# Performance work log

Measured on AMD Instinct MI355X. Metric: run time of the kernel, lower is better.

## Reference

```python
import jax, jax.numpy as jnp
import numpy as np

EPS = 1e-5
N, CIN, C = 8192, 64, 128
K_POS, K_LARGE, K_DOWN = 16, 127, 16

def _bn(h, g, b):
    # training-mode BatchNorm1d (biased var), as in the torch forward
    return (h - h.mean(0)) / jnp.sqrt(h.var(0) + EPS) * g + b

def _knn_idx(f, k):
    # k nearest neighbors per row (self excluded), grouped per target node
    sq = jnp.sum(f * f, axis=1)
    d = sq[:, None] + sq[None, :] - 2.0 * (f @ f.T)
    d = d.at[jnp.diag_indices(f.shape[0])].set(jnp.inf)
    return jax.lax.top_k(-d, k)[1]

def _fps(pos, m):
    # farthest point sampling, deterministic start at node 0; indices are non-diff
    pos = jax.lax.stop_gradient(pos)
    n = pos.shape[0]
    def step(carry, _):
        dist, last = carry
        dist = jnp.minimum(dist, jnp.sum((pos - pos[last]) ** 2, axis=1))
        nxt = jnp.argmax(dist).astype(jnp.int32)
        return (dist, nxt), nxt
    (_, _), rest = jax.lax.scan(step, (jnp.full((n,), jnp.inf), jnp.array(0, jnp.int32)), None, length=m - 1)
    return jnp.sort(jnp.concatenate([jnp.zeros((1,), jnp.int32), rest]))

def _lin(k, i, o):
    return jax.random.normal(k, (i, o), dtype=jnp.float32) / np.float32(np.sqrt(i))

def setup_inputs():
    ks = jax.random.split(jax.random.key(0), 16)
    return dict(
        x=jax.random.normal(ks[0], (N, CIN), dtype=jnp.float32),
        pos=jax.random.uniform(ks[1], (N, 3), dtype=jnp.float32),
        edge_index=jax.random.randint(ks[2], (2, N * 16), 0, N),
        Wd=_lin(ks[3], CIN, C), bd=jnp.zeros((C,)),
        gamma_d=jnp.ones((C,)), beta_d=jnp.zeros((C,)),
        Wg1=_lin(ks[4], C, C), bg1=jnp.zeros((C,)),
        gamma_g=jnp.ones((C,)), beta_g=jnp.zeros((C,)),
        Wg2=_lin(ks[5], C, 20), bg2=jnp.zeros((20,)),
        Wlin=_lin(ks[6], C, C), Wsrc=_lin(ks[7], C, C), Wdst=_lin(ks[8], C, C),
        Wp=_lin(ks[9], 3, C), bp=jnp.zeros((C,)),
        Wa1=_lin(ks[10], C, C), ba1=jnp.zeros((C,)),
        gamma_a=jnp.ones((C,)), beta_a=jnp.zeros((C,)),
        Wa2=_lin(ks[11], C, C), ba2=jnp.zeros((C,)),
        Wu=_lin(ks[12], C, C), bu=jnp.zeros((C,)),
    )

def reference(x, pos, edge_index, Wd, bd, gamma_d, beta_d, Wg1, bg1, gamma_g, beta_g,
              Wg2, bg2, Wlin, Wsrc, Wdst, Wp, bp, Wa1, ba1, gamma_a, beta_a, Wa2, ba2, Wu, bu):
    # ---- downlayer: Linear+BN+ReLU, neighbor max-pool (w/ self loop), FPS ----
    h = jax.nn.relu(_bn(x @ Wd + bd, gamma_d, beta_d))                 # [N,C]
    pooled = jax.ops.segment_max(h[edge_index[0]], edge_index[1], num_segments=N)
    pooled = jnp.maximum(pooled, h)                                     # add self loop
    idx = _fps(pos, N // 2)
    x1, pos1 = pooled[idx], pos[idx]                                    # [M,C],[M,3]
    M = N // 2
    # ---- generate_graph: pos kNN (k=16) + feature kNN (k=127) + gumbel top-k ----
    nn_pos = _knn_idx(pos1, K_POS)                                      # [M,16]
    e_pos_src = nn_pos.reshape(-1)
    e_pos_dst = jnp.repeat(jnp.arange(M), K_POS)
    nn_feat = _knn_idx(x1, K_LARGE)                                     # [M,127]
    src_l = nn_feat.reshape(-1)
    dst_l = jnp.repeat(jnp.arange(M), K_LARGE)
    hg = jax.nn.relu(_bn(x1 @ Wg1 + bg1, gamma_g, beta_g))
    emb = hg @ Wg2 + bg2                                                # [M,20]
    k1, k2 = jax.random.split(jax.random.key(42))
    emb = emb + jax.random.uniform(k1, emb.shape) * 1e-4
    dist = jnp.linalg.norm(emb[src_l] - emb[dst_l], axis=1)
    p = jnp.exp(-(dist ** 2)).reshape(M, K_LARGE)                       # t = 1.0
    g = -jnp.log(-jnp.log(jax.random.uniform(k2, p.shape) + 1e-20) + 1e-20)
    top_i = jax.lax.top_k(jnp.log(p + 1e-20) + g, K_DOWN)[1]            # [M,16]
    flat = (top_i + jnp.arange(M)[:, None] * K_LARGE).reshape(-1)
    s = jnp.concatenate([src_l[flat], e_pos_src])                       # [E=M*32]
    d = jnp.concatenate([dst_l[flat], e_pos_dst])
    # ---- PointTransformerConv + linear_up + residual ----
    a_src, a_dst, v = x1 @ Wsrc, x1 @ Wdst, x1 @ Wlin
    delta = (pos1[d] - pos1[s]) @ Wp + bp                               # [E,C]
    alpha = a_dst[d] - a_src[s] + delta
    alpha = jax.nn.relu(_bn(alpha @ Wa1 + ba1, gamma_a, beta_a)) @ Wa2 + ba2
    amax = jax.ops.segment_max(alpha, d, num_segments=M)                # per-target softmax
    ea = jnp.exp(alpha - amax[d])
    w = ea / (jax.ops.segment_sum(ea, d, num_segments=M)[d] + 1e-16)
    out = jax.ops.segment_sum(w * (v[s] + delta), d, num_segments=M)    # [M,C]
    return out @ Wu + bu + x1
```

## Files before the change

kernel.cpp:

```cpp
#include <hip/hip_runtime.h>
#include <cstdint>
#include <cstddef>
#include <math.h>

#define NNODE 8192
#define CINP 64
#define CC 128
#define MM 4096
#define KPOS 16
#define KLARGE 127
#define KDOWN 16
#define EG (MM*KDOWN)
#define ETOT (EG*2)
#define NEDGE 131072

__host__ __device__ static inline void tf_block(uint32_t k0, uint32_t k1,
                                                uint32_t c0, uint32_t c1,
                                                uint32_t& o0, uint32_t& o1) {
  uint32_t ks2 = k0 ^ k1 ^ 0x1BD11BDAu;
  uint32_t x0 = c0 + k0, x1 = c1 + k1;
#define TFR(r) { x0 += x1; x1 = (x1 << (r)) | (x1 >> (32 - (r))); x1 ^= x0; }
  TFR(13) TFR(15) TFR(26) TFR(6)
  x0 += k1;  x1 += ks2 + 1u;
  TFR(17) TFR(29) TFR(16) TFR(24)
  x0 += ks2; x1 += k0 + 2u;
  TFR(13) TFR(15) TFR(26) TFR(6)
  x0 += k0;  x1 += k1 + 3u;
  TFR(17) TFR(29) TFR(16) TFR(24)
  x0 += k1;  x1 += ks2 + 4u;
  TFR(13) TFR(15) TFR(26) TFR(6)
  x0 += ks2; x1 += k0 + 5u;
#undef TFR
  o0 = x0; o1 = x1;
}

__global__ void k_uniform(float* __restrict__ u, int n, uint32_t ka, uint32_t kb) {
  int i = blockIdx.x * 256 + threadIdx.x;
  if (i >= n) return;
  uint32_t o0, o1;
  tf_block(ka, kb, 0u, (uint32_t)i, o0, o1);
  uint32_t bits = o0 ^ o1;
  u[i] = __uint_as_float((bits >> 9) | 0x3f800000u) - 1.0f;
}

__global__ __launch_bounds__(256) void k_gemm32(const float* __restrict__ A, const float* __restrict__ B,
                                                const float* __restrict__ bias, float* __restrict__ Cmat, int rows) {
  int id = blockIdx.x * 256 + threadIdx.x;
  int r = id >> 7, c = id & (CC - 1);
  if (r >= rows) return;
  const float* a = A + r * CC;
  float acc = 0.f;
#pragma unroll 8
  for (int k = 0; k < CC; k++) acc = __fmaf_rn(a[k], B[k * CC + c], acc);
  if (bias) acc = __fadd_rn(acc, bias[c]);
  Cmat[id] = acc;
}

template<int K>
__global__ __launch_bounds__(256) void k_gemm64(const float* __restrict__ A, const float* __restrict__ B,
                                                const float* __restrict__ bias, float* __restrict__ Cmat, int rows) {
  int id = blockIdx.x * 256 + threadIdx.x;
  int r = id >> 7, c = id & (CC - 1);
  if (r >= rows) return;
  const float* a = A + r * K;
  double acc = 0.0;
#pragma unroll 4
  for (int k = 0; k < K; k++) acc += (double)a[k] * (double)B[k * CC + c];
  float v = (float)acc;
  if (bias) v = __fadd_rn(v, bias[c]);
  Cmat[id] = v;
}

__global__ __launch_bounds__(256) void k_gemm_res(const float* __restrict__ A, const float* __restrict__ B,
                                                  const float* __restrict__ bias, const float* __restrict__ res,
                                                  float* __restrict__ Cmat, int rows) {
  int id = blockIdx.x * 256 + threadIdx.x;
  int r = id >> 7, c = id & (CC - 1);
  if (r >= rows) return;
  const float* a = A + r * CC;
  float acc = 0.f;
#pragma unroll 8
  for (int k = 0; k < CC; k++) acc = __fmaf_rn(a[k], B[k * CC + c], acc);
  acc = __fadd_rn(acc, bias[c]);
  Cmat[id] = __fadd_rn(acc, res[id]);
}

__global__ __launch_bounds__(128) void k_colsum_part(const float* __restrict__ A, int rows, int rpb,
                                                     double* __restrict__ part) {
  int c = threadIdx.x, b = blockIdx.x;
  int r0 = b * rpb, r1 = r0 + rpb; if (r1 > rows) r1 = rows;
  double s = 0.0;
  for (int r = r0; r < r1; r++) s += (double)A[(size_t)r * CC + c];
  part[(size_t)b * CC + c] = s;
}
__global__ __launch_bounds__(128) void k_colmean(const double* __restrict__ part, int np, double rows,
                                                 float* __restrict__ mean) {
  int c = threadIdx.x;
  double s = 0.0;
  for (int b = 0; b < np; b++) s += part[(size_t)b * CC + c];
  mean[c] = (float)(s / rows);
}
__global__ __launch_bounds__(128) void k_colvar_part(const float* __restrict__ A, int rows, int rpb,
                                                     const float* __restrict__ mean, double* __restrict__ part) {
  int c = threadIdx.x, b = blockIdx.x;
  int r0 = b * rpb, r1 = r0 + rpb; if (r1 > rows) r1 = rows;
  float m32 = mean[c];
  double q = 0.0;
  for (int r = r0; r < r1; r++) {
    float d = __fsub_rn(A[(size_t)r * CC + c], m32);
    q += (double)d * (double)d;
  }
  part[(size_t)b * CC + c] = q;
}
__global__ __launch_bounds__(128) void k_colvar_fin(const double* __restrict__ part, int np, double rows,
                                                    float* __restrict__ var) {
  int c = threadIdx.x;
  double s = 0.0;
  for (int b = 0; b < np; b++) s += part[(size_t)b * CC + c];
  var[c] = (float)(s / rows);
}

__global__ __launch_bounds__(128) void k_colstat64(const float* __restrict__ A, int rows, int rpb,
                                                   double* __restrict__ dsum, double* __restrict__ dsq) {
  int c = threadIdx.x;
  int r0 = blockIdx.x * rpb;
  int r1 = r0 + rpb; if (r1 > rows) r1 = rows;
  double s = 0.0, q = 0.0;
  for (int r = r0; r < r1; r++) {
    float v = A[(size_t)r * CC + c];
    s += (double)v;
    q += (double)v * (double)v;
  }
  atomicAdd(&dsum[c], s);
  atomicAdd(&dsq[c], q);
}

__global__ __launch_bounds__(128) void k_finstat(const double* __restrict__ dsum, const double* __restrict__ dsq,
                                                 double rows, float* __restrict__ mean, float* __restrict__ var) {
  int c = threadIdx.x;
  double m = dsum[c] / rows;
  mean[c] = (float)m;
  var[c] = (float)(dsq[c] / rows - m * m);
}

__global__ void k_bnrelu(const float* __restrict__ in, const float* __restrict__ mean, const float* __restrict__ var,
                         const float* __restrict__ g, const float* __restrict__ b,
                         float* __restrict__ o1, float* __restrict__ o2, int total) {
  int id = blockIdx.x * 256 + threadIdx.x;
  if (id >= total) return;
  int c = id & (CC - 1);
  float sd = __fsqrt_rn(__fadd_rn(var[c], 1e-5f));
  float vv = __fdiv_rn(__fsub_rn(in[id], mean[c]), sd);
  vv = fmaxf(__fadd_rn(__fmul_rn(vv, g[c]), b[c]), 0.0f);
  o1[id] = vv;
  if (o2) o2[id] = vv;
}

__global__ void k_pool(const float* __restrict__ h, const int* __restrict__ ei, float* __restrict__ pooled) {
  int id = blockIdx.x * 256 + threadIdx.x;
  int e = id >> 7, c = id & (CC - 1);
  int src = ei[e], dst = ei[NEDGE + e];
  atomicMax((int*)(pooled + (size_t)dst * CC + c), __float_as_int(h[(size_t)src * CC + c]));
}

#define FPS_DPP_STEP(CTRL)                                                              \
  {                                                                                     \
    uint32_t nlo = (uint32_t)__builtin_amdgcn_update_dpp(0, (int)klo, CTRL, 0xf, 0xf, true); \
    uint32_t nhi = (uint32_t)__builtin_amdgcn_update_dpp(0, (int)khi, CTRL, 0xf, 0xf, true); \
    unsigned long long nk = ((unsigned long long)nhi << 32) | nlo;                      \
    unsigned long long ck = ((unsigned long long)khi << 32) | klo;                      \
    if (nk > ck) { klo = nlo; khi = nhi; }                                              \
  }

__global__ __launch_bounds__(512) void k_fps(const float* __restrict__ pos, int* __restrict__ idx) {
  constexpr int T = 512, P = 16;
  __shared__ unsigned int keys[NNODE];
  __shared__ float ldx[NNODE], ldy[NNODE], ldz[NNODE];
  __shared__ unsigned int sel[NNODE / 32];
  __shared__ int scn[T];
  __shared__ __align__(16) unsigned long long redk[2][8];
  int t = threadIdx.x;
  for (int i = t; i < NNODE; i += T) {
    float X = pos[3 * i], Y = pos[3 * i + 1], Z = pos[3 * i + 2];
    ldx[i] = X; ldy[i] = Y; ldz[i] = Z;
    int cx = (int)(X * 64.0f); cx = cx < 0 ? 0 : (cx > 63 ? 63 : cx);
    int cy = (int)(Y * 64.0f); cy = cy < 0 ? 0 : (cy > 63 ? 63 : cy);
    int cz = (int)(Z * 64.0f); cz = cz < 0 ? 0 : (cz > 63 ? 63 : cz);
    unsigned int code = 0;
    for (int b = 0; b < 6; b++) {
      code |= (unsigned)((cx >> b) & 1) << (3 * b + 2);
      code |= (unsigned)((cy >> b) & 1) << (3 * b + 1);
      code |= (unsigned)((cz >> b) & 1) << (3 * b);
    }
    keys[i] = (code << 13) | (unsigned)i;
  }
  for (int i = t; i < NNODE / 32; i += T) sel[i] = 0u;
  __syncthreads();
  for (int k = 2; k <= NNODE; k <<= 1) {
    for (int j = k >> 1; j > 0; j >>= 1) {
      for (int i = t; i < NNODE; i += T) {
        int l = i ^ j;
        if (l > i) {
          unsigned a = keys[i], b = keys[l];
          bool up = ((i & k) == 0);
          if ((a > b) == up) { keys[i] = b; keys[l] = a; }
        }
      }
      __syncthreads();
    }
  }
  float px[P], py[P], pz[P], dist[P];
  uint32_t invo[P];
  float bnx = 1e30f, bxx = -1e30f, bny = 1e30f, bxy = -1e30f, bnz = 1e30f, bxz = -1e30f;
#pragma unroll
  for (int j = 0; j < P; j++) {
    int i = (int)(keys[t * P + j] & 8191u);
    invo[j] = (uint32_t)(8191 - i);
    px[j] = ldx[i]; py[j] = ldy[i]; pz[j] = ldz[i];
    dist[j] = __int_as_float(0x7f800000);
    bnx = fminf(bnx, px[j]); bxx = fmaxf(bxx, px[j]);
    bny = fminf(bny, py[j]); bxy = fmaxf(bxy, py[j]);
    bnz = fminf(bnz, pz[j]); bxz = fmaxf(bxz, pz[j]);
  }
  if (t == 0) sel[0] = 1u;
  float Lx = ldx[0], Ly = ldy[0], Lz = ldz[0];
  float myMax = __int_as_float(0x7f800000);
  unsigned long long myKey = 0ull;
  int w = t >> 6, lane = t & 63;
  for (int it = 0; it < MM - 1; it++) {
    float cx = fminf(fmaxf(Lx, bnx), bxx);
    float cy = fminf(fmaxf(Ly, bny), bxy);
    float cz = fminf(fmaxf(Lz, bnz), bxz);
    float ddx = Lx - cx, ddy = Ly - cy, ddz = Lz - cz;
    float lb = ddx * ddx + ddy * ddy + ddz * ddz;
    if (lb * 0.98f - 1e-6f < myMax) {
      unsigned long long bk = 0ull;
#pragma unroll
      for (int j = 0; j < P; j++) {
        float dx = __fsub_rn(px[j], Lx), dy = __fsub_rn(py[j], Ly), dz = __fsub_rn(pz[j], Lz);
        float d2 = __fadd_rn(__fadd_rn(__fmul_rn(dx, dx), __fmul_rn(dy, dy)), __fmul_rn(dz, dz));
        float nd = fminf(dist[j], d2);
        dist[j] = nd;
        unsigned long long kj = ((unsigned long long)__float_as_uint(nd) << 13) | (unsigned long long)invo[j];
        if (kj > bk) bk = kj;
      }
      myKey = bk;
      myMax = __uint_as_float((uint32_t)(bk >> 13));
    }
    uint32_t klo = (uint32_t)myKey, khi = (uint32_t)(myKey >> 32);
    FPS_DPP_STEP(0x111)
    FPS_DPP_STEP(0x112)
    FPS_DPP_STEP(0x114)
    FPS_DPP_STEP(0x118)
    FPS_DPP_STEP(0x142)
    FPS_DPP_STEP(0x143)
    uint32_t wlo = (uint32_t)__builtin_amdgcn_readlane((int)klo, 63);
    uint32_t whi = (uint32_t)__builtin_amdgcn_readlane((int)khi, 63);
    unsigned long long wk = ((unsigned long long)whi << 32) | wlo;
    int p = it & 1;
    if (lane == 0) redk[p][w] = wk;
    __syncthreads();
    const ulonglong2* rp = (const ulonglong2*)&redk[p][0];
    ulonglong2 r0 = rp[0], r1 = rp[1], r2 = rp[2], r3 = rp[3];
    unsigned long long m0 = r0.x > r0.y ? r0.x : r0.y;
    unsigned long long m1 = r1.x > r1.y ? r1.x : r1.y;
    unsigned long long m2 = r2.x > r2.y ? r2.x : r2.y;
    unsigned long long m3 = r3.x > r3.y ? r3.x : r3.y;
    unsigned long long ga = m0 > m1 ? m0 : m1;
    unsigned long long gb = m2 > m3 ? m2 : m3;
    unsigned long long g = ga > gb ? ga : gb;
    int o = 8191 - (int)(g & 8191ull);
    Lx = ldx[o]; Ly = ldy[o]; Lz = ldz[o];
    if (t == 0) atomicOr((int*)&sel[o >> 5], (int)(1u << (o & 31)));
  }
  __syncthreads();
  int cnt = 0;
#pragma unroll
  for (int j = 0; j < P; j++) {
    int i = t * P + j;
    cnt += (int)((sel[i >> 5] >> (i & 31)) & 1u);
  }
  scn[t] = cnt;
  __syncthreads();
  for (int off = 1; off < T; off <<= 1) {
    int v = scn[t];
    int add = (t >= off) ? scn[t - off] : 0;
    __syncthreads();
    scn[t] = v + add;
    __syncthreads();
  }
  int p = scn[t] - cnt;
#pragma unroll
  for (int j = 0; j < P; j++) {
    int i = t * P + j;
    if ((sel[i >> 5] >> (i & 31)) & 1u) idx[p++] = i;
  }
}

__global__ __launch_bounds__(128) void k_gather(const float* __restrict__ pooled, const float* __restrict__ pos,
                                                const int* __restrict__ idxi, float* __restrict__ x1,
                                                float* __restrict__ x1T, float* __restrict__ pos1,
                                                double* __restrict__ sqp, double* __restrict__ sqf) {
  int m = blockIdx.x, t = threadIdx.x;
  int src = idxi[m];
  float v = pooled[(size_t)src * CC + t];
  x1[m * CC + t] = v;
  x1T[t * MM + m] = v;
  __shared__ double s2[CC];
  s2[t] = (double)v * (double)v;
  __syncthreads();
  if (t == 0) {
    double acc = 0.0;
    for (int i = 0; i < CC; i++) acc += s2[i];
    sqf[m] = acc;
    float X = pos[3 * src], Y = pos[3 * src + 1], Z = pos[3 * src + 2];
    pos1[3 * m] = X; pos1[3 * m + 1] = Y; pos1[3 * m + 2] = Z;
    sqp[m] = (double)X * X + (double)Y * Y + (double)Z * Z;
  }
}

__global__ __launch_bounds__(128) void k_knn_pos(const float* __restrict__ pos1, const double* __restrict__ sqp,
                                                 int* __restrict__ sedge) {
  int i = blockIdx.x, t = threadIdx.x;
  __shared__ float d[MM];
  __shared__ float rv[128];
  __shared__ int ri[128];
  double xi = pos1[3 * i], yi = pos1[3 * i + 1], zi = pos1[3 * i + 2], si = sqp[i];
  for (int j = t; j < MM; j += 128) {
    double dot = xi * (double)pos1[3 * j] + yi * (double)pos1[3 * j + 1] + zi * (double)pos1[3 * j + 2];
    float dd = (float)(si + sqp[j] - 2.0 * dot);
    d[j] = (j == i) ? __int_as_float(0x7f800000) : dd;
  }
  __syncthreads();
  for (int s = 0; s < KPOS; s++) {
    float bv = __int_as_float(0x7f800000); int bi = MM;
    for (int j = t; j < MM; j += 128) {
      float v = d[j];
      if (v < bv || (v == bv && j < bi)) { bv = v; bi = j; }
    }
    rv[t] = bv; ri[t] = bi;
    __syncthreads();
    if (t == 0) {
      for (int q = 1; q < 128; q++)
        if (rv[q] < rv[0] || (rv[q] == rv[0] && ri[q] < ri[0])) { rv[0] = rv[q]; ri[0] = ri[q]; }
      sedge[EG + i * KPOS + s] = ri[0];
      d[ri[0]] = __int_as_float(0x7f800000);
    }
    __syncthreads();
  }
}

__global__ __launch_bounds__(256) void k_dmat(const float* __restrict__ x1, const float* __restrict__ x1T,
                                              const double* __restrict__ sqf, float* __restrict__ D) {
  __shared__ float As2[16][128];
  int bid = blockIdx.x;
  int i0 = (bid >> 4) << 4;
  int j0 = (bid & 15) << 8;
  int t = threadIdx.x;
  for (int u = t; u < 16 * CC; u += 256) {
    int q = u >> 7, k = u & (CC - 1);
    As2[q][k] = x1[(i0 + q) * CC + k];
  }
  __syncthreads();
  int j = j0 + t;
  double sj = sqf[j];
#pragma unroll
  for (int pass = 0; pass < 2; pass++) {
    double acc[8];
#pragma unroll
    for (int q = 0; q < 8; q++) acc[q] = 0.0;
    for (int k = 0; k < CC; k++) {
      double bv = (double)x1T[k * MM + j];
#pragma unroll
      for (int q = 0; q < 8; q++) acc[q] += (double)As2[pass * 8 + q][k] * bv;
    }
#pragma unroll
    for (int q = 0; q < 8; q++) {
      int i = i0 + pass * 8 + q;
      float d = (float)(sqf[i] + sj - 2.0 * acc[q]);
      D[(size_t)i * MM + j] = (i == j) ? __int_as_float(0x7f800000) : d;
    }
  }
}

__global__ __launch_bounds__(256) void k_knn_feat(const float* __restrict__ D, int* __restrict__ nnf) {
  int tt = threadIdx.x;
  int lane = tt & 63, wid = tt >> 6;
  int i = blockIdx.x * 4 + wid;
  const float* drow = D + (size_t)i * MM;
  __shared__ float Lv[8][256];
  __shared__ int Lj[8][256];
  float lv[8]; int lj[8];
#pragma unroll
  for (int q = 0; q < 8; q++) { lv[q] = __int_as_float(0x7f800000); lj[q] = MM; }
  for (int tix = 0; tix < MM / 64; tix++) {
    int j = lane + (tix << 6);
    float v = drow[j];
    if (v < lv[7] || (v == lv[7] && j < lj[7])) {
      lv[7] = v; lj[7] = j;
#pragma unroll
      for (int q = 7; q >= 1; q--) {
        bool sw = (lv[q] < lv[q - 1]) || (lv[q] == lv[q - 1] && lj[q] < lj[q - 1]);
        if (sw) { float tv = lv[q]; lv[q] = lv[q - 1]; lv[q - 1] = tv;
                  int tj = lj[q]; lj[q] = lj[q - 1]; lj[q - 1] = tj; }
      }
    }
  }
#pragma unroll
  for (int q = 0; q < 8; q++) { Lv[q][tt] = lv[q]; Lj[q][tt] = lj[q]; }
  int hp = 0;
  for (int s = 0; s < KLARGE; s++) {
    float hv = (hp < 8) ? Lv[hp][tt] : __int_as_float(0x7f800000);
    int hj = (hp < 8) ? Lj[hp][tt] : MM;
    float bv = hv; int bj = hj;
#pragma unroll
    for (int off = 1; off < 64; off <<= 1) {
      float ov = __shfl_xor(bv, off);
      int oj = __shfl_xor(bj, off);
      if (ov < bv || (ov == bv && oj < bj)) { bv = ov; bj = oj; }
    }
    if (lane == 0) nnf[(size_t)i * KLARGE + s] = bj;
    if (bj < MM && (bj & 63) == lane) {
      hp++;
      if (hp == 8) {
        float nv[8]; int nj[8];
#pragma unroll
        for (int q = 0; q < 8; q++) { nv[q] = __int_as_float(0x7f800000); nj[q] = MM; }
        for (int tix = 0; tix < MM / 64; tix++) {
          int j = lane + (tix << 6);
          float v = drow[j];
          bool after = (v > bv) || (v == bv && j > bj);
          if (after && (v < nv[7] || (v == nv[7] && j < nj[7]))) {
            nv[7] = v; nj[7] = j;
#pragma unroll
            for (int q = 7; q >= 1; q--) {
              bool sw = (nv[q] < nv[q - 1]) || (nv[q] == nv[q - 1] && nj[q] < nj[q - 1]);
              if (sw) { float tv = nv[q]; nv[q] = nv[q - 1]; nv[q - 1] = tv;
                        int tj = nj[q]; nj[q] = nj[q - 1]; nj[q - 1] = tj; }
            }
          }
        }
#pragma unroll
        for (int q = 0; q < 8; q++) { Lv[q][tt] = nv[q]; Lj[q][tt] = nj[q]; }
        hp = 0;
      }
    }
  }
}

__global__ __launch_bounds__(64) void k_emb(const float* __restrict__ hg, const float* __restrict__ Wg2,
                                            const float* __restrict__ bg2, const float* __restrict__ u1,
                                            float* __restrict__ emb) {
  int m = blockIdx.x, t = threadIdx.x;
  if (t >= 20) return;
  double acc = 0.0;
  for (int k = 0; k < CC; k++) acc += (double)hg[m * CC + k] * (double)Wg2[k * 20 + t];
  float v = (float)acc;
  v = __fadd_rn(v, bg2[t]);
  v = __fadd_rn(v, __fmul_rn(u1[m * 20 + t], 1e-4f));
  emb[m * 20 + t] = v;
}

__global__ __launch_bounds__(128) void k_gumbel(const float* __restrict__ emb, const int* __restrict__ nnf,
                                                const float* __restrict__ u2, int* __restrict__ sedge) {
  int i = blockIdx.x, t = threadIdx.x;
  __shared__ float ei[20];
  __shared__ float sc[KLARGE];
  __shared__ int sj[KLARGE];
  if (t < 20) ei[t] = emb[i * 20 + t];
  __syncthreads();
  if (t < KLARGE) {
    int j = nnf[(size_t)i * KLARGE + t];
    double res = 0.0;
#pragma unroll
    for (int q = 0; q < 20; q++) {
      float df = __fsub_rn(ei[q], emb[j * 20 + q]);
      res += (double)df * (double)df;
    }
    float dist = (float)sqrt(res);
    float d2 = __fmul_rn(dist, dist);
    float p = expf(-d2);
    float u = u2[i * KLARGE + t];
    float inner = logf(__fadd_rn(u, 1e-20f));
    float g = -logf(__fadd_rn(-inner, 1e-20f));
    sc[t] = __fadd_rn(logf(__fadd_rn(p, 1e-20f)), g);
    sj[t] = j;
  }
  __syncthreads();
  if (t == 0) {
    for (int s = 0; s < KDOWN; s++) {
      float bv = -__int_as_float(0x7f800000); int bs = 0;
      for (int q = 0; q < KLARGE; q++)
        if (sc[q] > bv) { bv = sc[q]; bs = q; }
      sedge[i * KDOWN + s] = sj[bs];
      sc[bs] = -__int_as_float(0x7f800000);
    }
  }
}

__global__ __launch_bounds__(128) void k_bp1(const float* __restrict__ bp, const float* __restrict__ Wa1,
                                             const float* __restrict__ ba1, float* __restrict__ bp1) {
  int t = threadIdx.x;
  float acc = 0.f;
  for (int k = 0; k < CC; k++) acc = __fmaf_rn(bp[k], Wa1[k * CC + t], acc);
  bp1[t] = __fadd_rn(acc, ba1[t]);
}

__global__ __launch_bounds__(256) void k_alpha1_elw(const float* __restrict__ P, const float* __restrict__ Q,
                                                    const float* __restrict__ pos1, const int* __restrict__ sedge,
                                                    const float* __restrict__ Wp1, const float* __restrict__ bp1,
                                                    float* __restrict__ alpha) {
  int id = blockIdx.x * 256 + threadIdx.x;
  int e = id >> 7, t = id & (CC - 1);
  int tgt = (e < EG) ? (e >> 4) : ((e - EG) >> 4);
  int src = sedge[e];
  float dpx = __fsub_rn(pos1[3 * tgt], pos1[3 * src]);
  float dpy = __fsub_rn(pos1[3 * tgt + 1], pos1[3 * src + 1]);
  float dpz = __fsub_rn(pos1[3 * tgt + 2], pos1[3 * src + 2]);
  float v = P[(size_t)tgt * CC + t] - Q[(size_t)src * CC + t];
  v = __fmaf_rn(dpx, Wp1[t], v);
  v = __fmaf_rn(dpy, Wp1[CC + t], v);
  v = __fmaf_rn(dpz, Wp1[2 * CC + t], v);
  alpha[(size_t)id] = __fadd_rn(v, bp1[t]);
}

__global__ __launch_bounds__(256) void k_alpha2_gemm(const float* __restrict__ alpha_in,
                                                     float* __restrict__ alpha_out,
                                                     const float* __restrict__ mean, const float* __restrict__ var,
                                                     const float* __restrict__ g, const float* __restrict__ b,
                                                     const float* __restrict__ Wa2, const float* __restrict__ ba2) {
  __shared__ float As[16][132];
  __shared__ float Bs[16][132];
  __shared__ float scl[CC], shf[CC];
  int t = threadIdx.x;
  int e0 = blockIdx.x * 128;
  if (t < CC) {
    float sd = __fsqrt_rn(__fadd_rn(var[t], 1e-5f));
    float s = __fdiv_rn(g[t], sd);
    scl[t] = s;
    shf[t] = __fsub_rn(b[t], __fmul_rn(mean[t], s));
  }
  int te = t >> 4, tc = t & 15;
  float acc[8][8];
#pragma unroll
  for (int ii = 0; ii < 8; ii++)
#pragma unroll
    for (int jj = 0; jj < 8; jj++) acc[ii][jj] = 0.f;
  for (int kc = 0; kc < CC; kc += 16) {
    __syncthreads();
    for (int u = t; u < 16 * 128; u += 256) {
      int ee = u >> 4, kk = u & 15;
      float a = alpha_in[(size_t)(e0 + ee) * CC + kc + kk];
      int k = kc + kk;
      As[kk][ee] = fmaxf(__fmaf_rn(a, scl[k], shf[k]), 0.f);
    }
    for (int u = t; u < 16 * 128; u += 256) {
      int kk = u >> 7, c = u & 127;
      Bs[kk][c] = Wa2[(kc + kk) * CC + c];
    }
    __syncthreads();
#pragma unroll
    for (int kk = 0; kk < 16; kk++) {
      float av[8], bv[8];
      *(float4*)&av[0] = *(const float4*)&As[kk][te * 8];
      *(float4*)&av[4] = *(const float4*)&As[kk][te * 8 + 4];
      *(float4*)&bv[0] = *(const float4*)&Bs[kk][tc * 8];
      *(float4*)&bv[4] = *(const float4*)&Bs[kk][tc * 8 + 4];
#pragma unroll
      for (int ii = 0; ii < 8; ii++)
#pragma unroll
        for (int jj = 0; jj < 8; jj++) acc[ii][jj] = __fmaf_rn(av[ii], bv[jj], acc[ii][jj]);
    }
  }
#pragma unroll
  for (int ii = 0; ii < 8; ii++) {
    int e = e0 + te * 8 + ii;
#pragma unroll
    for (int jj = 0; jj < 8; jj++) {
      int c = tc * 8 + jj;
      alpha_out[(size_t)e * CC + c] = __fadd_rn(acc[ii][jj], ba2[c]);
    }
  }
}

__global__ __launch_bounds__(128) void k_outagg(const float* __restrict__ alpha, const float* __restrict__ vmat,
                                                const float* __restrict__ pos1, const int* __restrict__ sedge,
                                                const float* __restrict__ Wp, const float* __restrict__ bp,
                                                float* __restrict__ outb) {
  int m = blockIdx.x, t = threadIdx.x;
  float al[32], dl[32]; int sr[32];
  float amax = -__int_as_float(0x7f800000);
  float pmx = pos1[3 * m], pmy = pos1[3 * m + 1], pmz = pos1[3 * m + 2];
  float wp0 = Wp[t], wp1 = Wp[CC + t], wp2 = Wp[2 * CC + t], bpt = bp[t];
#pragma unroll
  for (int e = 0; e < 32; e++) {
    int row = (e < 16) ? (m * 16 + e) : (EG + m * 16 + (e - 16));
    int src = sedge[row];
    sr[e] = src;
    float a = alpha[(size_t)row * CC + t];
    al[e] = a;
    amax = fmaxf(amax, a);
    float d0 = __fsub_rn(pmx, pos1[3 * src]);
    float d1 = __fsub_rn(pmy, pos1[3 * src + 1]);
    float d2 = __fsub_rn(pmz, pos1[3 * src + 2]);
    float del = __fmaf_rn(d2, wp2, __fmaf_rn(d1, wp1, __fmul_rn(d0, wp0)));
    dl[e] = __fadd_rn(del, bpt);
  }
  float s1 = 0.f, s2 = 0.f;
#pragma unroll
  for (int e = 0; e < 32; e++) {
    float ea = expf(__fsub_rn(al[e], amax));
    s1 = __fadd_rn(s1, ea);
    float val = __fadd_rn(vmat[sr[e] * CC + t], dl[e]);
    s2 = __fmaf_rn(ea, val, s2);
  }
  outb[m * CC + t] = __fdiv_rn(s2, __fadd_rn(s1, 1e-16f));
}

extern "C" void kernel_launch(void* const* d_in, const int* in_sizes, int n_in,
                              void* d_out, int out_size, void* d_ws, size_t ws_size,
                              hipStream_t stream) {
  (void)in_sizes; (void)n_in; (void)out_size; (void)ws_size;
  const float* x    = (const float*)d_in[0];
  const float* pos  = (const float*)d_in[1];
  const int*   ei   = (const int*)d_in[2];
  const float* Wd   = (const float*)d_in[3];
  const float* bd   = (const float*)d_in[4];
  const float* gd   = (const float*)d_in[5];
  const float* btd  = (const float*)d_in[6];
  const float* Wg1  = (const float*)d_in[7];
  const float* bg1  = (const float*)d_in[8];
  const float* gg   = (const float*)d_in[9];
  const float* btg  = (const float*)d_in[10];
  const float* Wg2  = (const float*)d_in[11];
  const float* bg2  = (const float*)d_in[12];
  const float* Wlin = (const float*)d_in[13];
  const float* Wsrc = (const float*)d_in[14];
  const float* Wdst = (const float*)d_in[15];
  const float* Wp   = (const float*)d_in[16];
  const float* bp   = (const float*)d_in[17];
  const float* Wa1  = (const float*)d_in[18];
  const float* ba1  = (const float*)d_in[19];
  const float* ga   = (const float*)d_in[20];
  const float* bta  = (const float*)d_in[21];
  const float* Wa2  = (const float*)d_in[22];
  const float* ba2  = (const float*)d_in[23];
  const float* Wu   = (const float*)d_in[24];
  const float* bu   = (const float*)d_in[25];
  float* out = (float*)d_out;

  char* ws = (char*)d_ws;
  double* dsum = (double*)(ws + 0);
  double* dsq  = (double*)(ws + 1024);
  float* fmean = (float*)(ws + 2048);
  float* fvar  = (float*)(ws + 2560);
  float* BIG   = (float*)(ws + 4096);
  size_t off = 4096 + (size_t)16777216 * 4;
  auto alloc = [&](size_t nbytes) { void* p = ws + off; off += (nbytes + 255) & ~(size_t)255; return p; };
  float* h_lin  = (float*)alloc((size_t)NNODE * CC * 4);
  float* h      = (float*)alloc((size_t)NNODE * CC * 4);
  float* pooled = (float*)alloc((size_t)NNODE * CC * 4);
  float* x1     = (float*)alloc((size_t)MM * CC * 4);
  float* x1T    = (float*)alloc((size_t)MM * CC * 4);
  float* hgl    = (float*)alloc((size_t)MM * CC * 4);
  float* hg     = (float*)alloc((size_t)MM * CC * 4);
  float* Pm     = (float*)alloc((size_t)MM * CC * 4);
  float* Qm     = (float*)alloc((size_t)MM * CC * 4);
  float* vmat   = (float*)alloc((size_t)MM * CC * 4);
  float* outb   = (float*)alloc((size_t)MM * CC * 4);
  float* pos1   = (float*)alloc((size_t)MM * 3 * 4);
  double* sqp   = (double*)alloc((size_t)MM * 8);
  double* sqf   = (double*)alloc((size_t)MM * 8);
  float* emb    = (float*)alloc((size_t)MM * 20 * 4);
  float* u1     = (float*)alloc(81920 * 4);
  float* u2     = (float*)alloc(520192 * 4);
  int* idxi     = (int*)alloc(MM * 4);
  int* nnf      = (int*)alloc((size_t)MM * KLARGE * 4);
  int* sedge    = (int*)alloc(ETOT * 4);
  double* partA = (double*)alloc(64 * CC * 8);
  double* partB = (double*)alloc(64 * CC * 8);
  float* Wdst1  = (float*)alloc(CC * CC * 4);
  float* Wsrc1  = (float*)alloc(CC * CC * 4);
  float* Wp1    = (float*)alloc(3 * CC * 4);
  float* bp1    = (float*)alloc(CC * 4);

  uint32_t o0, o1, k1a, k1b, k2a, k2b;
  tf_block(0u, 42u, 0u, 0u, o0, o1); k1a = o0; k1b = o1;
  tf_block(0u, 42u, 0u, 1u, o0, o1); k2a = o0; k2b = o1;

  k_gemm64<CINP><<<dim3(NNODE * CC / 256), dim3(256), 0, stream>>>(x, Wd, bd, h_lin, NNODE);
  k_colsum_part<<<dim3(64), dim3(128), 0, stream>>>(h_lin, NNODE, 128, partA);
  k_colmean<<<dim3(1), dim3(128), 0, stream>>>(partA, 64, (double)NNODE, fmean);
  k_colvar_part<<<dim3(64), dim3(128), 0, stream>>>(h_lin, NNODE, 128, fmean, partB);
  k_colvar_fin<<<dim3(1), dim3(128), 0, stream>>>(partB, 64, (double)NNODE, fvar);
  k_bnrelu<<<dim3(NNODE * CC / 256), dim3(256), 0, stream>>>(h_lin, fmean, fvar, gd, btd, h, pooled, NNODE * CC);
  k_pool<<<dim3(NEDGE * CC / 256), dim3(256), 0, stream>>>(h, ei, pooled);
  k_fps<<<dim3(1), dim3(512), 0, stream>>>(pos, idxi);
  k_gather<<<dim3(MM), dim3(128), 0, stream>>>(pooled, pos, idxi, x1, x1T, pos1, sqp, sqf);

  k_knn_pos<<<dim3(MM), dim3(128), 0, stream>>>(pos1, sqp, sedge);
  k_dmat<<<dim3(4096), dim3(256), 0, stream>>>(x1, x1T, sqf, BIG);
  k_knn_feat<<<dim3(MM / 4), dim3(256), 0, stream>>>(BIG, nnf);
  k_gemm64<CC><<<dim3(MM * CC / 256), dim3(256), 0, stream>>>(x1, Wg1, bg1, hgl, MM);
  k_colsum_part<<<dim3(32), dim3(128), 0, stream>>>(hgl, MM, 128, partA);
  k_colmean<<<dim3(1), dim3(128), 0, stream>>>(partA, 32, (double)MM, fmean);
  k_colvar_part<<<dim3(32), dim3(128), 0, stream>>>(hgl, MM, 128, fmean, partB);
  k_colvar_fin<<<dim3(1), dim3(128), 0, stream>>>(partB, 32, (double)MM, fvar);
  k_bnrelu<<<dim3(MM * CC / 256), dim3(256), 0, stream>>>(hgl, fmean, fvar, gg, btg, hg, (float*)nullptr, MM * CC);
  k_uniform<<<dim3((81920 + 255) / 256), dim3(256), 0, stream>>>(u1, 81920, k1a, k1b);
  k_uniform<<<dim3((520192 + 255) / 256), dim3(256), 0, stream>>>(u2, 520192, k2a, k2b);
  k_emb<<<dim3(MM), dim3(64), 0, stream>>>(hg, Wg2, bg2, u1, emb);
  k_gumbel<<<dim3(MM), dim3(128), 0, stream>>>(emb, nnf, u2, sedge);

  k_gemm32<<<dim3(CC * CC / 256), dim3(256), 0, stream>>>(Wdst, Wa1, (const float*)nullptr, Wdst1, CC);
  k_gemm32<<<dim3(CC * CC / 256), dim3(256), 0, stream>>>(Wsrc, Wa1, (const float*)nullptr, Wsrc1, CC);
  k_gemm32<<<dim3(2), dim3(256), 0, stream>>>(Wp, Wa1, (const float*)nullptr, Wp1, 3);
  k_bp1<<<dim3(1), dim3(128), 0, stream>>>(bp, Wa1, ba1, bp1);
  k_gemm32<<<dim3(MM * CC / 256), dim3(256), 0, stream>>>(x1, Wdst1, (const float*)nullptr, Pm, MM);
  k_gemm32<<<dim3(MM * CC / 256), dim3(256), 0, stream>>>(x1, Wsrc1, (const float*)nullptr, Qm, MM);
  k_gemm32<<<dim3(MM * CC / 256), dim3(256), 0, stream>>>(x1, Wlin, (const float*)nullptr, vmat, MM);
  k_alpha1_elw<<<dim3(ETOT * CC / 256), dim3(256), 0, stream>>>(Pm, Qm, pos1, sedge, Wp1, bp1, BIG);
  hipMemsetAsync(ws, 0, 2048, stream);
  k_colstat64<<<dim3(256), dim3(128), 0, stream>>>(BIG, ETOT, 512, dsum, dsq);
  k_finstat<<<dim3(1), dim3(128), 0, stream>>>(dsum, dsq, (double)ETOT, fmean, fvar);
  k_alpha2_gemm<<<dim3(ETOT / 128), dim3(256), 0, stream>>>(BIG, BIG, fmean, fvar, ga, bta, Wa2, ba2);
  k_outagg<<<dim3(MM), dim3(128), 0, stream>>>(BIG, vmat, pos1, sedge, Wp, bp, outb);
  k_gemm_res<<<dim3(MM * CC / 256), dim3(256), 0, stream>>>(outb, Wu, bu, x1, out, MM);
}
```

Baseline: 5.437 ms.

## Overlap serial FPS with independent front work in one launch; DPP-reduce kNN

Folds the single-block farthest-point-sampling kernel, the input linear layer, the uniform RNG generation, and the weight-premultiply GEMMs into one heterogeneous launch. Block 0 runs FPS while the other blocks do work that does not depend on it, so the long serial FPS loop overlaps with that work instead of running alone. Separately, the positional kNN selection replaces the single-thread 128-way argmin with a packed 64-bit key reduction using DPP wavefront ops and a two-wave combine. The trade-off is that the fused launch's runtime is bounded by the FPS block, and the dependent BN kernels now wait for FPS to finish.

```diff
diff --git a/kernel.cpp b/kernel.cpp
--- a/kernel.cpp
+++ b/kernel.cpp
@@ -34,15 +34,6 @@
   o0 = x0; o1 = x1;
 }
 
-__global__ void k_uniform(float* __restrict__ u, int n, uint32_t ka, uint32_t kb) {
-  int i = blockIdx.x * 256 + threadIdx.x;
-  if (i >= n) return;
-  uint32_t o0, o1;
-  tf_block(ka, kb, 0u, (uint32_t)i, o0, o1);
-  uint32_t bits = o0 ^ o1;
-  u[i] = __uint_as_float((bits >> 9) | 0x3f800000u) - 1.0f;
-}
-
 __global__ __launch_bounds__(256) void k_gemm32(const float* __restrict__ A, const float* __restrict__ B,
                                                 const float* __restrict__ bias, float* __restrict__ Cmat, int rows) {
   int id = blockIdx.x * 256 + threadIdx.x;
@@ -172,128 +163,224 @@
     if (nk > ck) { klo = nlo; khi = nhi; }                                              \
   }
 
-__global__ __launch_bounds__(512) void k_fps(const float* __restrict__ pos, int* __restrict__ idx) {
-  constexpr int T = 512, P = 16;
-  __shared__ unsigned int keys[NNODE];
-  __shared__ float ldx[NNODE], ldy[NNODE], ldz[NNODE];
-  __shared__ unsigned int sel[NNODE / 32];
-  __shared__ int scn[T];
-  __shared__ __align__(16) unsigned long long redk[2][8];
-  int t = threadIdx.x;
-  for (int i = t; i < NNODE; i += T) {
-    float X = pos[3 * i], Y = pos[3 * i + 1], Z = pos[3 * i + 2];
-    ldx[i] = X; ldy[i] = Y; ldz[i] = Z;
-    int cx = (int)(X * 64.0f); cx = cx < 0 ? 0 : (cx > 63 ? 63 : cx);
-    int cy = (int)(Y * 64.0f); cy = cy < 0 ? 0 : (cy > 63 ? 63 : cy);
-    int cz = (int)(Z * 64.0f); cz = cz < 0 ? 0 : (cz > 63 ? 63 : cz);
-    unsigned int code = 0;
-    for (int b = 0; b < 6; b++) {
-      code |= (unsigned)((cx >> b) & 1) << (3 * b + 2);
-      code |= (unsigned)((cy >> b) & 1) << (3 * b + 1);
-      code |= (unsigned)((cz >> b) & 1) << (3 * b);
-    }
-    keys[i] = (code << 13) | (unsigned)i;
-  }
-  for (int i = t; i < NNODE / 32; i += T) sel[i] = 0u;
-  __syncthreads();
-  for (int k = 2; k <= NNODE; k <<= 1) {
-    for (int j = k >> 1; j > 0; j >>= 1) {
-      for (int i = t; i < NNODE; i += T) {
-        int l = i ^ j;
-        if (l > i) {
-          unsigned a = keys[i], b = keys[l];
-          bool up = ((i & k) == 0);
-          if ((a > b) == up) { keys[i] = b; keys[l] = a; }
+#define KNN_DPP_MIN_STEP(CTRL)                                                          \
+  {                                                                                     \
+    uint32_t nlo = (uint32_t)__builtin_amdgcn_update_dpp(-1, (int)klo, CTRL, 0xf, 0xf, false); \
+    uint32_t nhi = (uint32_t)__builtin_amdgcn_update_dpp(-1, (int)khi, CTRL, 0xf, 0xf, false); \
+    unsigned long long nk = ((unsigned long long)nhi << 32) | nlo;                      \
+    unsigned long long ck = ((unsigned long long)khi << 32) | klo;                      \
+    if (nk < ck) { klo = nlo; khi = nhi; }                                              \
+  }
+
+#define FB_HL   2049
+#define FB_U1   2209
+#define FB_U2   3225
+#define FB_W1   3257
+#define FB_W2   3289
+#define FB_WP   3289
+#define FB_BP   3290
+#define FB_GRID 3291
+
+__global__ __launch_bounds__(512) void k_front(const float* __restrict__ pos, int* __restrict__ idx,
+                                               const float* __restrict__ x, const float* __restrict__ Wd,
+                                               const float* __restrict__ bd, float* __restrict__ h_lin,
+                                               float* __restrict__ u1, float* __restrict__ u2,
+                                               uint32_t k1a, uint32_t k1b, uint32_t k2a, uint32_t k2b,
+                                               const float* __restrict__ Wdst, const float* __restrict__ Wsrc,
+                                               const float* __restrict__ Wa1, const float* __restrict__ Wp,
+                                               const float* __restrict__ bp, const float* __restrict__ ba1,
+                                               float* __restrict__ Wdst1, float* __restrict__ Wsrc1,
+                                               float* __restrict__ Wp1, float* __restrict__ bp1) {
+  int bid = blockIdx.x, t = threadIdx.x;
+  if (bid == 0) {
+    constexpr int T = 512, P = 16;
+    __shared__ unsigned int keys[NNODE];
+    __shared__ float ldx[NNODE], ldy[NNODE], ldz[NNODE];
+    __shared__ unsigned int sel[NNODE / 32];
+    __shared__ int scn[T];
+    __shared__ __align__(16) unsigned long long redk[2][8];
+    for (int i = t; i < NNODE; i += T) {
+      float X = pos[3 * i], Y = pos[3 * i + 1], Z = pos[3 * i + 2];
+      ldx[i] = X; ldy[i] = Y; ldz[i] = Z;
+      int cx = (int)(X * 64.0f); cx = cx < 0 ? 0 : (cx > 63 ? 63 : cx);
+      int cy = (int)(Y * 64.0f); cy = cy < 0 ? 0 : (cy > 63 ? 63 : cy);
+      int cz = (int)(Z * 64.0f); cz = cz < 0 ? 0 : (cz > 63 ? 63 : cz);
+      unsigned int code = 0;
+      for (int b = 0; b < 6; b++) {
+        code |= (unsigned)((cx >> b) & 1) << (3 * b + 2);
+        code |= (unsigned)((cy >> b) & 1) << (3 * b + 1);
+        code |= (unsigned)((cz >> b) & 1) << (3 * b);
+      }
+      keys[i] = (code << 13) | (unsigned)i;
+    }
+    for (int i = t; i < NNODE / 32; i += T) sel[i] = 0u;
+    __syncthreads();
+    for (int k = 2; k <= NNODE; k <<= 1) {
+      for (int j = k >> 1; j > 0; j >>= 1) {
+        for (int i = t; i < NNODE; i += T) {
+          int l = i ^ j;
+          if (l > i) {
+            unsigned a = keys[i], b = keys[l];
+            bool up = ((i & k) == 0);
+            if ((a > b) == up) { keys[i] = b; keys[l] = a; }
+          }
         }
+        __syncthreads();
       }
+    }
+    float px[P], py[P], pz[P], dist[P];
+    uint32_t invo[P];
+    float bnx = 1e30f, bxx = -1e30f, bny = 1e30f, bxy = -1e30f, bnz = 1e30f, bxz = -1e30f;
+#pragma unroll
+    for (int j = 0; j < P; j++) {
+      int i = (int)(keys[t * P + j] & 8191u);
+      invo[j] = (uint32_t)(8191 - i);
+      px[j] = ldx[i]; py[j] = ldy[i]; pz[j] = ldz[i];
+      dist[j] = __int_as_float(0x7f800000);
+      bnx = fminf(bnx, px[j]); bxx = fmaxf(bxx, px[j]);
+      bny = fminf(bny, py[j]); bxy = fmaxf(bxy, py[j]);
+      bnz = fminf(bnz, pz[j]); bxz = fmaxf(bxz, pz[j]);
+    }
+    if (t == 0) sel[0] = 1u;
+    float Lx = ldx[0], Ly = ldy[0], Lz = ldz[0];
+    float myMax = __int_as_float(0x7f800000);
+    unsigned long long myKey = 0ull;
+    int w = t >> 6, lane = t & 63;
+    __syncthreads();
+    for (int it = 0; it < MM - 1; it++) {
+      float cx = fminf(fmaxf(Lx, bnx), bxx);
+      float cy = fminf(fmaxf(Ly, bny), bxy);
+      float cz = fminf(fmaxf(Lz, bnz), bxz);
+      float ddx = Lx - cx, ddy = Ly - cy, ddz = Lz - cz;
+      float lb = ddx * ddx + ddy * ddy + ddz * ddz;
+      if (lb * 0.98f - 1e-6f < myMax) {
+        unsigned long long bk = 0ull;
+#pragma unroll
+        for (int j = 0; j < P; j++) {
+          float dx = __fsub_rn(px[j], Lx), dy = __fsub_rn(py[j], Ly), dz = __fsub_rn(pz[j], Lz);
+          float d2 = __fadd_rn(__fadd_rn(__fmul_rn(dx, dx), __fmul_rn(dy, dy)), __fmul_rn(dz, dz));
+          float nd = fminf(dist[j], d2);
+          dist[j] = nd;
+          unsigned long long kj = ((unsigned long long)__float_as_uint(nd) << 13) | (unsigned long long)invo[j];
+          if (kj > bk) bk = kj;
+        }
+        myKey = bk;
+        myMax = __uint_as_float((uint32_t)(bk >> 13));
+      }
+      uint32_t klo = (uint32_t)myKey, khi = (uint32_t)(myKey >> 32);
+      FPS_DPP_STEP(0x111)
+      FPS_DPP_STEP(0x112)
+      FPS_DPP_STEP(0x114)
+      FPS_DPP_STEP(0x118)
+      FPS_DPP_STEP(0x142)
+      FPS_DPP_STEP(0x143)
+      uint32_t wlo = (uint32_t)__builtin_amdgcn_readlane((int)klo, 63);
+      uint32_t whi = (uint32_t)__builtin_amdgcn_readlane((int)khi, 63);
+      unsigned long long wk = ((unsigned long long)whi << 32) | wlo;
+      int p = it & 1;
+      if (lane == 0) redk[p][w] = wk;
       __syncthreads();
-    }
-  }
-  float px[P], py[P], pz[P], dist[P];
-  uint32_t invo[P];
-  float bnx = 1e30f, bxx = -1e30f, bny = 1e30f, bxy = -1e30f, bnz = 1e30f, bxz = -1e30f;
-#pragma unroll
-  for (int j = 0; j < P; j++) {
-    int i = (int)(keys[t * P + j] & 8191u);
-    invo[j] = (uint32_t)(8191 - i);
-    px[j] = ldx[i]; py[j] = ldy[i]; pz[j] = ldz[i];
-    dist[j] = __int_as_float(0x7f800000);
-    bnx = fminf(bnx, px[j]); bxx = fmaxf(bxx, px[j]);
-    bny = fminf(bny, py[j]); bxy = fmaxf(bxy, py[j]);
-    bnz = fminf(bnz, pz[j]); bxz = fmaxf(bxz, pz[j]);
-  }
-  if (t == 0) sel[0] = 1u;
-  float Lx = ldx[0], Ly = ldy[0], Lz = ldz[0];
-  float myMax = __int_as_float(0x7f800000);
-  unsigned long long myKey = 0ull;
-  int w = t >> 6, lane = t & 63;
-  for (int it = 0; it < MM - 1; it++) {
-    float cx = fminf(fmaxf(Lx, bnx), bxx);
-    float cy = fminf(fmaxf(Ly, bny), bxy);
-    float cz = fminf(fmaxf(Lz, bnz), bxz);
-    float ddx = Lx - cx, ddy = Ly - cy, ddz = Lz - cz;
-    float lb = ddx * ddx + ddy * ddy + ddz * ddz;
-    if (lb * 0.98f - 1e-6f < myMax) {
-      unsigned long long bk = 0ull;
-#pragma unroll
-      for (int j = 0; j < P; j++) {
-        float dx = __fsub_rn(px[j], Lx), dy = __fsub_rn(py[j], Ly), dz = __fsub_rn(pz[j], Lz);
-        float d2 = __fadd_rn(__fadd_rn(__fmul_rn(dx, dx), __fmul_rn(dy, dy)), __fmul_rn(dz, dz));
-        float nd = fminf(dist[j], d2);
-        dist[j] = nd;
-        unsigned long long kj = ((unsigned long long)__float_as_uint(nd) << 13) | (unsigned long long)invo[j];
-        if (kj > bk) bk = kj;
-      }
-      myKey = bk;
-      myMax = __uint_as_float((uint32_t)(bk >> 13));
-    }
-    uint32_t klo = (uint32_t)myKey, khi = (uint32_t)(myKey >> 32);
-    FPS_DPP_STEP(0x111)
-    FPS_DPP_STEP(0x112)
-    FPS_DPP_STEP(0x114)
-    FPS_DPP_STEP(0x118)
-    FPS_DPP_STEP(0x142)
-    FPS_DPP_STEP(0x143)
-    uint32_t wlo = (uint32_t)__builtin_amdgcn_readlane((int)klo, 63);
-    uint32_t whi = (uint32_t)__builtin_amdgcn_readlane((int)khi, 63);
-    unsigned long long wk = ((unsigned long long)whi << 32) | wlo;
-    int p = it & 1;
-    if (lane == 0) redk[p][w] = wk;
+      const ulonglong2* rp = (const ulonglong2*)&redk[p][0];
+      ulonglong2 r0 = rp[0], r1 = rp[1], r2 = rp[2], r3 = rp[3];
+      unsigned long long m0 = r0.x > r0.y ? r0.x : r0.y;
+      unsigned long long m1 = r1.x > r1.y ? r1.x : r1.y;
+      unsigned long long m2 = r2.x > r2.y ? r2.x : r2.y;
+      unsigned long long m3 = r3.x > r3.y ? r3.x : r3.y;
+      unsigned long long ga = m0 > m1 ? m0 : m1;
+      unsigned long long gb = m2 > m3 ? m2 : m3;
+      unsigned long long g = ga > gb ? ga : gb;
+      int o = 8191 - (int)(g & 8191ull);
+      Lx = ldx[o]; Ly = ldy[o]; Lz = ldz[o];
+      if (t == 0) atomicOr((int*)&sel[o >> 5], (int)(1u << (o & 31)));
+    }
     __syncthreads();
-    const ulonglong2* rp = (const ulonglong2*)&redk[p][0];
-    ulonglong2 r0 = rp[0], r1 = rp[1], r2 = rp[2], r3 = rp[3];
-    unsigned long long m0 = r0.x > r0.y ? r0.x : r0.y;
-    unsigned long long m1 = r1.x > r1.y ? r1.x : r1.y;
-    unsigned long long m2 = r2.x > r2.y ? r2.x : r2.y;
-    unsigned long long m3 = r3.x > r3.y ? r3.x : r3.y;
-    unsigned long long ga = m0 > m1 ? m0 : m1;
-    unsigned long long gb = m2 > m3 ? m2 : m3;
-    unsigned long long g = ga > gb ? ga : gb;
-    int o = 8191 - (int)(g & 8191ull);
-    Lx = ldx[o]; Ly = ldy[o]; Lz = ldz[o];
-    if (t == 0) atomicOr((int*)&sel[o >> 5], (int)(1u << (o & 31)));
-  }
-  __syncthreads();
-  int cnt = 0;
-#pragma unroll
-  for (int j = 0; j < P; j++) {
-    int i = t * P + j;
-    cnt += (int)((sel[i >> 5] >> (i & 31)) & 1u);
-  }
-  scn[t] = cnt;
-  __syncthreads();
-  for (int off = 1; off < T; off <<= 1) {
-    int v = scn[t];
-    int add = (t >= off) ? scn[t - off] : 0;
+    int cnt = 0;
+#pragma unroll
+    for (int j = 0; j < P; j++) {
+      int i = t * P + j;
+      cnt += (int)((sel[i >> 5] >> (i & 31)) & 1u);
+    }
+    scn[t] = cnt;
     __syncthreads();
-    scn[t] = v + add;
-    __syncthreads();
-  }
-  int p = scn[t] - cnt;
-#pragma unroll
-  for (int j = 0; j < P; j++) {
-    int i = t * P + j;
-    if ((sel[i >> 5] >> (i & 31)) & 1u) idx[p++] = i;
+    for (int off = 1; off < T; off <<= 1) {
+      int v = scn[t];
+      int add = (t >= off) ? scn[t - off] : 0;
+      __syncthreads();
+      scn[t] = v + add;
+      __syncthreads();
+    }
+    int p = scn[t] - cnt;
+#pragma unroll
+    for (int j = 0; j < P; j++) {
+      int i = t * P + j;
+      if ((sel[i >> 5] >> (i & 31)) & 1u) idx[p++] = i;
+    }
+    return;
+  }
+  if (bid < FB_HL) {
+    int id = (bid - 1) * 512 + t;
+    int r = id >> 7, c = id & (CC - 1);
+    const float* a = x + r * CINP;
+    double acc = 0.0;
+#pragma unroll 4
+    for (int k = 0; k < CINP; k++) acc += (double)a[k] * (double)Wd[k * CC + c];
+    float v = (float)acc;
+    v = __fadd_rn(v, bd[c]);
+    h_lin[id] = v;
+    return;
+  }
+  if (bid < FB_U1) {
+    int i = (bid - FB_HL) * 512 + t;
+    if (i < 81920) {
+      uint32_t o0, o1;
+      tf_block(k1a, k1b, 0u, (uint32_t)i, o0, o1);
+      uint32_t bits = o0 ^ o1;
+      u1[i] = __uint_as_float((bits >> 9) | 0x3f800000u) - 1.0f;
+    }
+    return;
+  }
+  if (bid < FB_U2) {
+    int i = (bid - FB_U1) * 512 + t;
+    if (i < 520192) {
+      uint32_t o0, o1;
+      tf_block(k2a, k2b, 0u, (uint32_t)i, o0, o1);
+      uint32_t bits = o0 ^ o1;
+      u2[i] = __uint_as_float((bits >> 9) | 0x3f800000u) - 1.0f;
+    }
+    return;
+  }
+  if (bid < FB_W1) {
+    int id = (bid - FB_U2) * 512 + t;
+    int r = id >> 7, c = id & (CC - 1);
+    float acc = 0.f;
+#pragma unroll 8
+    for (int k = 0; k < CC; k++) acc = __fmaf_rn(Wdst[r * CC + k], Wa1[k * CC + c], acc);
+    Wdst1[id] = acc;
+    return;
+  }
+  if (bid < FB_W2) {
+    int id = (bid - FB_W1) * 512 + t;
+    int r = id >> 7, c = id & (CC - 1);
+    float acc = 0.f;
+#pragma unroll 8
+    for (int k = 0; k < CC; k++) acc = __fmaf_rn(Wsrc[r * CC + k], Wa1[k * CC + c], acc);
+    Wsrc1[id] = acc;
+    return;
+  }
+  if (bid == FB_WP) {
+    if (t < 3 * CC) {
+      int r = t >> 7, c = t & (CC - 1);
+      float acc = 0.f;
+#pragma unroll 8
+      for (int k = 0; k < CC; k++) acc = __fmaf_rn(Wp[r * CC + k], Wa1[k * CC + c], acc);
+      Wp1[t] = acc;
+    }
+    return;
+  }
+  if (t < CC) {
+    float acc = 0.f;
+    for (int k = 0; k < CC; k++) acc = __fmaf_rn(bp[k], Wa1[k * CC + t], acc);
+    bp1[t] = __fadd_rn(acc, ba1[t]);
   }
 }
 
@@ -323,8 +410,7 @@
                                                  int* __restrict__ sedge) {
   int i = blockIdx.x, t = threadIdx.x;
   __shared__ float d[MM];
-  __shared__ float rv[128];
-  __shared__ int ri[128];
+  __shared__ __align__(16) unsigned long long rr[2][2];
   double xi = pos1[3 * i], yi = pos1[3 * i + 1], zi = pos1[3 * i + 2], si = sqp[i];
   for (int j = t; j < MM; j += 128) {
     double dot = xi * (double)pos1[3 * j] + yi * (double)pos1[3 * j + 1] + zi * (double)pos1[3 * j + 2];
@@ -332,20 +418,32 @@
     d[j] = (j == i) ? __int_as_float(0x7f800000) : dd;
   }
   __syncthreads();
+  int lane = t & 63, w = t >> 6;
   for (int s = 0; s < KPOS; s++) {
-    float bv = __int_as_float(0x7f800000); int bi = MM;
+    unsigned long long best = ~0ull;
     for (int j = t; j < MM; j += 128) {
-      float v = d[j];
-      if (v < bv || (v == bv && j < bi)) { bv = v; bi = j; }
-    }
-    rv[t] = bv; ri[t] = bi;
+      uint32_t fb = __float_as_uint(d[j]);
+      fb = (fb & 0x80000000u) ? ~fb : (fb | 0x80000000u);
+      unsigned long long key = ((unsigned long long)fb << 13) | (unsigned long long)(unsigned)j;
+      if (key < best) best = key;
+    }
+    uint32_t klo = (uint32_t)best, khi = (uint32_t)(best >> 32);
+    KNN_DPP_MIN_STEP(0x111)
+    KNN_DPP_MIN_STEP(0x112)
+    KNN_DPP_MIN_STEP(0x114)
+    KNN_DPP_MIN_STEP(0x118)
+    KNN_DPP_MIN_STEP(0x142)
+    KNN_DPP_MIN_STEP(0x143)
+    uint32_t wlo = (uint32_t)__builtin_amdgcn_readlane((int)klo, 63);
+    uint32_t whi = (uint32_t)__builtin_amdgcn_readlane((int)khi, 63);
+    unsigned long long wk = ((unsigned long long)whi << 32) | wlo;
+    int p = s & 1;
+    if (lane == 0) rr[p][w] = wk;
     __syncthreads();
-    if (t == 0) {
-      for (int q = 1; q < 128; q++)
-        if (rv[q] < rv[0] || (rv[q] == rv[0] && ri[q] < ri[0])) { rv[0] = rv[q]; ri[0] = ri[q]; }
-      sedge[EG + i * KPOS + s] = ri[0];
-      d[ri[0]] = __int_as_float(0x7f800000);
-    }
+    unsigned long long g = rr[p][0] < rr[p][1] ? rr[p][0] : rr[p][1];
+    int bi = (int)(g & 8191ull);
+    if (t == 0) sedge[EG + i * KPOS + s] = bi;
+    if (t == (bi & 127)) d[bi] = __int_as_float(0x7f800000);
     __syncthreads();
   }
 }
@@ -496,14 +594,6 @@
       sc[bs] = -__int_as_float(0x7f800000);
     }
   }
-}
-
-__global__ __launch_bounds__(128) void k_bp1(const float* __restrict__ bp, const float* __restrict__ Wa1,
-                                             const float* __restrict__ ba1, float* __restrict__ bp1) {
-  int t = threadIdx.x;
-  float acc = 0.f;
-  for (int k = 0; k < CC; k++) acc = __fmaf_rn(bp[k], Wa1[k * CC + t], acc);
-  bp1[t] = __fadd_rn(acc, ba1[t]);
 }
 
 __global__ __launch_bounds__(256) void k_alpha1_elw(const float* __restrict__ P, const float* __restrict__ Q,
@@ -688,14 +778,17 @@
   tf_block(0u, 42u, 0u, 0u, o0, o1); k1a = o0; k1b = o1;
   tf_block(0u, 42u, 0u, 1u, o0, o1); k2a = o0; k2b = o1;
 
-  k_gemm64<CINP><<<dim3(NNODE * CC / 256), dim3(256), 0, stream>>>(x, Wd, bd, h_lin, NNODE);
+  k_front<<<dim3(FB_GRID), dim3(512), 0, stream>>>(pos, idxi, x, Wd, bd, h_lin,
+                                                   u1, u2, k1a, k1b, k2a, k2b,
+                                                   Wdst, Wsrc, Wa1, Wp, bp, ba1,
+                                                   Wdst1, Wsrc1, Wp1, bp1);
+
   k_colsum_part<<<dim3(64), dim3(128), 0, stream>>>(h_lin, NNODE, 128, partA);
   k_colmean<<<dim3(1), dim3(128), 0, stream>>>(partA, 64, (double)NNODE, fmean);
   k_colvar_part<<<dim3(64), dim3(128), 0, stream>>>(h_lin, NNODE, 128, fmean, partB);
   k_colvar_fin<<<dim3(1), dim3(128), 0, stream>>>(partB, 64, (double)NNODE, fvar);
   k_bnrelu<<<dim3(NNODE * CC / 256), dim3(256), 0, stream>>>(h_lin, fmean, fvar, gd, btd, h, pooled, NNODE * CC);
   k_pool<<<dim3(NEDGE * CC / 256), dim3(256), 0, stream>>>(h, ei, pooled);
-  k_fps<<<dim3(1), dim3(512), 0, stream>>>(pos, idxi);
   k_gather<<<dim3(MM), dim3(128), 0, stream>>>(pooled, pos, idxi, x1, x1T, pos1, sqp, sqf);
 
   k_knn_pos<<<dim3(MM), dim3(128), 0, stream>>>(pos1, sqp, sedge);
@@ -707,15 +800,9 @@
   k_colvar_part<<<dim3(32), dim3(128), 0, stream>>>(hgl, MM, 128, fmean, partB);
   k_colvar_fin<<<dim3(1), dim3(128), 0, stream>>>(partB, 32, (double)MM, fvar);
   k_bnrelu<<<dim3(MM * CC / 256), dim3(256), 0, stream>>>(hgl, fmean, fvar, gg, btg, hg, (float*)nullptr, MM * CC);
-  k_uniform<<<dim3((81920 + 255) / 256), dim3(256), 0, stream>>>(u1, 81920, k1a, k1b);
-  k_uniform<<<dim3((520192 + 255) / 256), dim3(256), 0, stream>>>(u2, 520192, k2a, k2b);
   k_emb<<<dim3(MM), dim3(64), 0, stream>>>(hg, Wg2, bg2, u1, emb);
   k_gumbel<<<dim3(MM), dim3(128), 0, stream>>>(emb, nnf, u2, sedge);
 
-  k_gemm32<<<dim3(CC * CC / 256), dim3(256), 0, stream>>>(Wdst, Wa1, (const float*)nullptr, Wdst1, CC);
-  k_gemm32<<<dim3(CC * CC / 256), dim3(256), 0, stream>>>(Wsrc, Wa1, (const float*)nullptr, Wsrc1, CC);
-  k_gemm32<<<dim3(2), dim3(256), 0, stream>>>(Wp, Wa1, (const float*)nullptr, Wp1, 3);
-  k_bp1<<<dim3(1), dim3(128), 0, stream>>>(bp, Wa1, ba1, bp1);
   k_gemm32<<<dim3(MM * CC / 256), dim3(256), 0, stream>>>(x1, Wdst1, (const float*)nullptr, Pm, MM);
   k_gemm32<<<dim3(MM * CC / 256), dim3(256), 0, stream>>>(x1, Wsrc1, (const float*)nullptr, Qm, MM);
   k_gemm32<<<dim3(MM * CC / 256), dim3(256), 0, stream>>>(x1, Wlin, (const float*)nullptr, vmat, MM);
```

Measured after the change: 5.031 ms. 7.5% less time.
